# Kernel tuning notes

Measured on AMD Instinct MI355X. Metric: run time of the kernel, lower is better.

Reference implementation:

```python
import jax, jax.numpy as jnp
import numpy as np

B, DIM, H, W = 2, 512, 48, 48
HEADS = 8
HD = DIM // HEADS
NS = 7
R = NS // 2
SCALE = HD ** -0.5
EPS = 1e-12


def _proj(x, w, b):
    # 1x1 conv == channel linear: x [B,C,H,W], w [O,C], b [O]
    return jnp.einsum('bchw,oc->bohw', x, w) + b[None, :, None, None]


def _to_heads(t):
    # [B,C,H,W] -> [B,heads,H,W,head_dim]
    return t.reshape(B, HEADS, HD, H, W).transpose(0, 1, 3, 4, 2)


def setup_inputs() -> dict:
    key = jax.random.key(0)
    ks = jax.random.split(key, 9)
    std = DIM ** -0.5
    inp = {'x': jax.random.normal(ks[0], (B, DIM, H, W), jnp.float32)}
    names = ['wq', 'bq', 'wk', 'bk', 'wv', 'bv', 'wo', 'bo']
    for i, n in enumerate(names):
        if n.startswith('w'):
            inp[n] = jax.random.normal(ks[i + 1], (DIM, DIM), jnp.float32) * std
        else:
            inp[n] = jnp.zeros((DIM,), jnp.float32)
    return inp


def reference(x, wq, bq, wk, bk, wv, bv, wo, bo):
    q = _proj(x, wq, bq)
    k = _proj(x, wk, bk)
    v = _proj(x, wv, bv)
    qh, kh, vh = _to_heads(q), _to_heads(k), _to_heads(v)

    offs = jnp.arange(-R, R + 1)
    oy, ox = jnp.meshgrid(offs, offs, indexing='ij')
    oy, ox = oy.reshape(-1), ox.reshape(-1)  # [K]
    by, bx = jnp.meshgrid(jnp.arange(H), jnp.arange(W), indexing='ij')
    ny = by[..., None] + oy  # [H,W,K]
    nx = bx[..., None] + ox
    valid = (ny >= 0) & (ny < H) & (nx >= 0) & (nx < W)  # [H,W,K]
    ny = jnp.clip(ny, 0, H - 1)
    nx = jnp.clip(nx, 0, W - 1)

    K = NS * NS
    T = H * W
    # gather neighborhoods: [B,heads,H,W,K,head_dim]
    k_nb = kh[:, :, ny, nx].reshape(B, HEADS, T, K, HD)
    v_nb = vh[:, :, ny, nx].reshape(B, HEADS, T, K, HD)
    q_tok = qh.reshape(B, HEADS, T, HD)

    scores = jnp.einsum('bhtd,bhtkd->bhtk', q_tok, k_nb) * SCALE
    neg = jnp.finfo(scores.dtype).min
    scores = jnp.where(valid.reshape(1, 1, T, K), scores, neg)
    attn = jax.nn.softmax(scores, axis=-1)
    out = jnp.einsum('bhtk,bhtkd->bhtd', attn, v_nb)

    # exclude self-value component (self-attention path)
    sv = vh.reshape(B, HEADS, T, HD)
    sv_unit = sv / jnp.maximum(jnp.linalg.norm(sv, axis=-1, keepdims=True), EPS)
    out = out - (out * sv_unit).sum(-1, keepdims=True) * sv_unit

    # [B,heads,T,HD] -> [B,C,H,W]
    out = out.reshape(B, HEADS, H, W, HD).transpose(0, 1, 4, 2, 3).reshape(B, DIM, H, W)
    return _proj(out, wo, bo)
```

## Files before the change

### kernel.cpp

```cpp
#include <hip/hip_runtime.h>
#include <hip/hip_bf16.h>
#include <math.h>

typedef __hip_bfloat16 bf16;
typedef __attribute__((ext_vector_type(4))) float f32x4;
typedef __attribute__((ext_vector_type(8))) short s16x8;
typedef __attribute__((ext_vector_type(4))) short s16x4;

#define B_     2
#define DIM_   512
#define Hh     48
#define Ww     48
#define T_     2304
#define HEADS_ 8
#define HD_    64
#define NS_    7
#define R_     3
#define KK_    49

#define LDSTR  40

__device__ __forceinline__ short f2bs(float f) {
    bf16 h = __float2bfloat16(f);
    return *(short*)&h;
}

__device__ __forceinline__ s16x8 cvt8(const float* __restrict__ p) {
    f32x4 a = *(const f32x4*)p;
    f32x4 b = *(const f32x4*)(p + 4);
    s16x8 r;
    r[0] = f2bs(a[0]); r[1] = f2bs(a[1]); r[2] = f2bs(a[2]); r[3] = f2bs(a[3]);
    r[4] = f2bs(b[0]); r[5] = f2bs(b[1]); r[6] = f2bs(b[2]); r[7] = f2bs(b[3]);
    return r;
}

__global__ __launch_bounds__(256) void wcvt(
    const float* __restrict__ wq, const float* __restrict__ wk,
    const float* __restrict__ wv, const float* __restrict__ wo,
    bf16* __restrict__ wb)
{
    const int i     = blockIdx.x * 256 + threadIdx.x;
    const int which = i >> 15;
    const int off   = (i & 32767) * 8;
    const float* src = (which == 0) ? wq : (which == 1) ? wk : (which == 2) ? wv : wo;
    *(s16x8*)((short*)wb + which * 262144 + off) = cvt8(src + off);
}

__global__ __launch_bounds__(256) void prep_xt(
    const float* __restrict__ x, bf16* __restrict__ xt)
{
    __shared__ short tile[64 * 72];
    const int t0 = blockIdx.x * 64;
    const int c0 = blockIdx.y * 64;
    const int b  = blockIdx.z;
    const int tid = threadIdx.x;

    const float* X = x + (size_t)b * DIM_ * T_;

    const int c_l = tid >> 4;
    const int t4  = (tid & 15) * 4;
#pragma unroll
    for (int cp = 0; cp < 4; ++cp) {
        const int c = cp * 16 + c_l;
        f32x4 v = *(const f32x4*)(X + (size_t)(c0 + c) * T_ + t0 + t4);
#pragma unroll
        for (int e = 0; e < 4; ++e) tile[(t4 + e) * 72 + c] = f2bs(v[e]);
    }
    __syncthreads();

    const int t_l = tid >> 2;
    const int c16 = (tid & 3) * 16;
    short* dst = (short*)xt + ((size_t)b * T_ + t0 + t_l) * DIM_ + c0 + c16;
    *(s16x8*)(dst)     = *(const s16x8*)(&tile[t_l * 72 + c16]);
    *(s16x8*)(dst + 8) = *(const s16x8*)(&tile[t_l * 72 + c16 + 8]);
}

__global__ __launch_bounds__(256) void gemm_qkv(
    const bf16* __restrict__ xt, const bf16* __restrict__ wb,
    const float* __restrict__ bq, const float* __restrict__ bk,
    const float* __restrict__ bv,
    bf16* __restrict__ qb2, bf16* __restrict__ kb2,
    float* __restrict__ vtf, bf16* __restrict__ vb2)
{
    const int tt   = blockIdx.x * 128;
    const int ot   = blockIdx.y * 64;
    const int b    = blockIdx.z;
    const int proj = ot >> 9;
    const int orow = ot & 511;
    const int head = orow >> 6;

    const float* bsel = (proj == 0) ? bq : (proj == 1) ? bk : bv;
    const short* Wb   = (const short*)wb + proj * 262144;

    const short* X = (const short*)xt + (size_t)b * T_ * DIM_;

    __shared__ __align__(16) short Xs[128 * LDSTR];
    __shared__ __align__(16) short Ws[64 * LDSTR];

    const int tid  = threadIdx.x;
    const int lane = tid & 63;
    const int wid  = tid >> 6;

    const int row = tid >> 2;
    const int cq  = (tid & 3) * 8;

    f32x4 acc[2][4];
#pragma unroll
    for (int r = 0; r < 2; ++r)
#pragma unroll
        for (int n = 0; n < 4; ++n) acc[r][n] = (f32x4){0.f, 0.f, 0.f, 0.f};

    for (int kk = 0; kk < DIM_; kk += 32) {
#pragma unroll
        for (int rr = 0; rr < 2; ++rr)
            *(s16x8*)(&Xs[(rr * 64 + row) * LDSTR + cq]) =
                *(const s16x8*)(X + (size_t)(tt + rr * 64 + row) * DIM_ + kk + cq);
        *(s16x8*)(&Ws[row * LDSTR + cq]) =
            *(const s16x8*)(Wb + (size_t)(orow + row) * DIM_ + kk + cq);
        __syncthreads();

        s16x8 a[2];
#pragma unroll
        for (int r = 0; r < 2; ++r)
            a[r] = *(const s16x8*)(&Xs[(r * 64 + wid * 16 + (lane & 15)) * LDSTR + 8 * (lane >> 4)]);
#pragma unroll
        for (int n = 0; n < 4; ++n) {
            s16x8 bf = *(const s16x8*)(&Ws[(n * 16 + (lane & 15)) * LDSTR + 8 * (lane >> 4)]);
#pragma unroll
            for (int r = 0; r < 2; ++r)
                acc[r][n] = __builtin_amdgcn_mfma_f32_16x16x32_bf16(a[r], bf, acc[r][n], 0, 0, 0);
        }
        __syncthreads();
    }

    const size_t hb = (size_t)(b * HEADS_ + head) * T_ * HD_;
    if (proj < 2) {
        short* ob = (short*)(proj == 0 ? qb2 : kb2) + hb;
#pragma unroll
        for (int r = 0; r < 2; ++r)
#pragma unroll
            for (int n = 0; n < 4; ++n) {
                const int d    = n * 16 + (lane & 15);
                const float bi = bsel[orow + d];
#pragma unroll
                for (int e = 0; e < 4; ++e) {
                    const int t = tt + r * 64 + wid * 16 + (lane >> 4) * 4 + e;
                    ob[(size_t)t * HD_ + d] = f2bs(acc[r][n][e] + bi);
                }
            }
    } else {
        float* of = vtf + hb;
        short* ob = (short*)vb2 + hb;
#pragma unroll
        for (int r = 0; r < 2; ++r)
#pragma unroll
            for (int n = 0; n < 4; ++n) {
                const int d    = n * 16 + (lane & 15);
                const float bi = bsel[orow + d];
#pragma unroll
                for (int e = 0; e < 4; ++e) {
                    const int t = tt + r * 64 + wid * 16 + (lane >> 4) * 4 + e;
                    const float vv = acc[r][n][e] + bi;
                    of[(size_t)t * HD_ + d] = vv;
                    ob[(size_t)t * HD_ + d] = f2bs(vv);
                }
            }
    }
}

__global__ __launch_bounds__(256) void gemm_out(
    const bf16* __restrict__ ao, const bf16* __restrict__ wb,
    const float* __restrict__ bo, float* __restrict__ out)
{
    const int tt = blockIdx.x * 64;
    const int ot = blockIdx.y * 64;
    const int b  = blockIdx.z;

    const short* X  = (const short*)ao + (size_t)b * T_ * DIM_;
    const short* Wb = (const short*)wb + 3 * 262144;

    __shared__ __align__(16) short Ws[64 * LDSTR];
    __shared__ __align__(16) short Xs[64 * LDSTR];

    const int tid  = threadIdx.x;
    const int lane = tid & 63;
    const int wid  = tid >> 6;

    const int row = tid >> 2;
    const int cq  = (tid & 3) * 8;

    f32x4 acc[4];
#pragma unroll
    for (int n = 0; n < 4; ++n) acc[n] = (f32x4){0.f, 0.f, 0.f, 0.f};

    for (int kk = 0; kk < DIM_; kk += 32) {
        *(s16x8*)(&Ws[row * LDSTR + cq]) =
            *(const s16x8*)(Wb + (size_t)(ot + row) * DIM_ + kk + cq);
        *(s16x8*)(&Xs[row * LDSTR + cq]) =
            *(const s16x8*)(X + (size_t)(tt + row) * DIM_ + kk + cq);
        __syncthreads();

        s16x8 a = *(const s16x8*)(&Ws[(wid * 16 + (lane & 15)) * LDSTR + 8 * (lane >> 4)]);
#pragma unroll
        for (int n = 0; n < 4; ++n) {
            s16x8 bf = *(const s16x8*)(&Xs[(n * 16 + (lane & 15)) * LDSTR + 8 * (lane >> 4)]);
            acc[n] = __builtin_amdgcn_mfma_f32_16x16x32_bf16(a, bf, acc[n], 0, 0, 0);
        }
        __syncthreads();
    }

    float* obase = out + (size_t)b * DIM_ * T_;
#pragma unroll
    for (int n = 0; n < 4; ++n) {
        const int t = tt + n * 16 + (lane & 15);
#pragma unroll
        for (int e = 0; e < 4; ++e) {
            const int o    = ot + wid * 16 + (lane >> 4) * 4 + e;
            obase[(size_t)o * T_ + t] = acc[n][e] + bo[o];
        }
    }
}

__global__ __launch_bounds__(256, 4) void attn_mfma(
    const bf16* __restrict__ qb2, const bf16* __restrict__ kb2,
    const float* __restrict__ vtf, const bf16* __restrict__ vb2,
    bf16* __restrict__ ao)
{
    __shared__ __align__(16) char smem[34048];
    short* Kl = (short*)smem;
    short* Ql = (short*)(smem + 25344);
    short* VT = (short*)smem;
    short* Pl = (short*)(smem + 27648);
    float* Ol = (float*)(smem + 27648);

    const int l   = blockIdx.x;
    const int idx = (l & 7) * 288 + (l >> 3);
    const int bh  = idx / 144;
    const int rem = idx - bh * 144;
    const int y   = rem / 3;
    const int x0  = (rem % 3) * 16;

    const short* qb  = (const short*)qb2 + (size_t)bh * T_ * HD_;
    const short* kb  = (const short*)kb2 + (size_t)bh * T_ * HD_;
    const short* vbb = (const short*)vb2 + (size_t)bh * T_ * HD_;
    const float* vbf = vtf + (size_t)bh * T_ * HD_;

    const int tid  = threadIdx.x;
    const int lane = tid & 63;
    const int wv   = tid >> 6;
    const int qq   = lane >> 4;
    const int ln   = lane & 15;

    if (tid < 32) {
        const int t = tid >> 1, c = tid & 1;
        *(s16x8*)&Pl[t * 200 + 176 + c * 8] = (s16x8){0,0,0,0,0,0,0,0};
    }
    {
        const int c8 = (tid & 7) * 8;
        const int wr = tid >> 3;
#pragma unroll
        for (int p = 0; p < 6; ++p) {
            const int w = p * 32 + wr;
            if (w < 168) {
                const int wy = w / 24, u = w - wy * 24;
                if (u < 22) {
                    const int gy = min(max(y + wy - 3, 0), 47);
                    const int gx = min(max(x0 + u - 3, 0), 47);
                    *(s16x8*)&Kl[w * 72 + c8] =
                        *(const s16x8*)(kb + (size_t)(gy * 48 + gx) * 64 + c8);
                }
            }
        }
    }
    if (tid < 128) {
        const int t = tid >> 3, c8 = (tid & 7) * 8;
        *(s16x8*)&Ql[t * 72 + c8] =
            *(const s16x8*)(qb + (size_t)(y * 48 + x0 + t) * 64 + c8);
    }
    s16x4 vreg[10];
    {
        const int rr0 = tid >> 4;
        const int d4  = (tid & 15) * 4;
#pragma unroll
        for (int p = 0; p < 10; ++p) {
            const int rr = p * 16 + rr0;
            if (rr < 154) {
                const int wy = rr / 22, u = rr - wy * 22;
                const int gy = min(max(y + wy - 3, 0), 47);
                const int gx = min(max(x0 + u - 3, 0), 47);
                vreg[p] = *(const s16x4*)(vbb + (size_t)(gy * 48 + gx) * 64 + d4);
            }
        }
    }
    __syncthreads();

    f32x4 acc[11];
#pragma unroll
    for (int mt = 0; mt < 11; ++mt) acc[mt] = (f32x4){0.f, 0.f, 0.f, 0.f};
#pragma unroll
    for (int ks = 0; ks < 2; ++ks) {
        s16x8 bq_ = *(const s16x8*)&Ql[ln * 72 + ks * 32 + qq * 8];
#pragma unroll
        for (int mt = 0; mt < 11; ++mt) {
            s16x8 ak = *(const s16x8*)&Kl[(mt * 16 + ln) * 72 + ks * 32 + qq * 8];
            acc[mt] = __builtin_amdgcn_mfma_f32_16x16x32_bf16(ak, bq_, acc[mt], 0, 0, 0);
        }
    }

    const int dx = ln;
    float mxv = -3.0e38f;
#pragma unroll
    for (int mt = 0; mt < 11; ++mt) {
#pragma unroll
        for (int e = 0; e < 4; ++e) {
            const int w  = mt * 16 + qq * 4 + e;
            const int wy = w / 24, u = w - wy * 24;
            const bool valid = (w < 168) &&
                               ((unsigned)(u - dx) <= 6u) &&
                               ((unsigned)(y + wy - 3) < 48u) &&
                               ((unsigned)(x0 + u - 3) < 48u);
            const float s = valid ? acc[mt][e] * 0.125f : -3.0e38f;
            acc[mt][e] = s;
            mxv = fmaxf(mxv, s);
        }
    }
    mxv = fmaxf(mxv, __shfl_xor(mxv, 16));
    mxv = fmaxf(mxv, __shfl_xor(mxv, 32));
    float sum = 0.f;
#pragma unroll
    for (int mt = 0; mt < 11; ++mt)
#pragma unroll
        for (int e = 0; e < 4; ++e) {
            const float p = __expf(acc[mt][e] - mxv);
            acc[mt][e] = p;
            sum += p;
        }
    sum += __shfl_xor(sum, 16);
    sum += __shfl_xor(sum, 32);
    const float inv = 1.0f / sum;

#pragma unroll
    for (int mt = 0; mt < 11; ++mt) {
        const int owner = (mt >= 9) ? 3 : (mt / 3);
        if (wv == owner) {
#pragma unroll
            for (int e = 0; e < 4; ++e) {
                const int w = mt * 16 + qq * 4 + e;
                Pl[ln * 200 + w] = f2bs(acc[mt][e] * inv);
            }
        }
    }
    __syncthreads();

    {
        const int d = tid >> 2, c = tid & 3;
        *(s16x8*)&VT[d * 200 + 168 + c * 8] = (s16x8){0,0,0,0,0,0,0,0};
    }
#pragma unroll
    for (int pp = 0; pp < 2; ++pp) {
        const int r2 = pp * 256 + tid;
        if (r2 < 448) {
            const int wy = r2 >> 6, d = r2 & 63;
            *(unsigned*)&VT[d * 200 + wy * 24 + 22] = 0u;
        }
    }
    {
        const int rr0 = tid >> 4;
        const int d4  = (tid & 15) * 4;
        const int rot = tid & 3;
#pragma unroll
        for (int p = 0; p < 10; ++p) {
            const int rr = p * 16 + rr0;
            if (rr < 154) {
                const int wy = rr / 22, u = rr - wy * 22;
                const int w  = wy * 24 + u;
#pragma unroll
                for (int e = 0; e < 4; ++e) {
                    const int ee = (e + rot) & 3;
                    VT[(d4 + ee) * 200 + w] = vreg[p][ee];
                }
            }
        }
    }
    __syncthreads();

    f32x4 oacc = (f32x4){0.f, 0.f, 0.f, 0.f};
#pragma unroll
    for (int ks = 0; ks < 6; ++ks) {
        s16x8 ap  = *(const s16x8*)&Pl[ln * 200 + ks * 32 + qq * 8];
        s16x8 bv_ = *(const s16x8*)&VT[(wv * 16 + ln) * 200 + ks * 32 + qq * 8];
        oacc = __builtin_amdgcn_mfma_f32_16x16x32_bf16(ap, bv_, oacc, 0, 0, 0);
    }
    __syncthreads();
#pragma unroll
    for (int e = 0; e < 4; ++e)
        Ol[(qq * 4 + e) * 72 + wv * 16 + ln] = oacc[e];
    __syncthreads();

    {
        const int tt = tid >> 4;
        const int dl = tid & 15;
        const int tg = y * 48 + x0 + tt;
        const float o0 = Ol[tt * 72 + dl],      o1 = Ol[tt * 72 + dl + 16],
                    o2 = Ol[tt * 72 + dl + 32], o3 = Ol[tt * 72 + dl + 48];
        const float* vs = vbf + (size_t)tg * 64 + dl;
        const float v0 = vs[0], v1 = vs[16], v2 = vs[32], v3 = vs[48];
        float n2  = v0 * v0 + v1 * v1 + v2 * v2 + v3 * v3;
        float odv = o0 * v0 + o1 * v1 + o2 * v2 + o3 * v3;
#pragma unroll
        for (int off = 1; off < 16; off <<= 1) {
            n2  += __shfl_xor(n2, off);
            odv += __shfl_xor(odv, off);
        }
        const float mxn = fmaxf(sqrtf(n2), 1e-12f);
        const float cf  = odv / (mxn * mxn);
        const int b = bh >> 3, h = bh & 7;
        bf16* dst = ao + ((size_t)b * T_ + tg) * DIM_ + h * 64 + dl;
        dst[0]  = __float2bfloat16(o0 - cf * v0);
        dst[16] = __float2bfloat16(o1 - cf * v1);
        dst[32] = __float2bfloat16(o2 - cf * v2);
        dst[48] = __float2bfloat16(o3 - cf * v3);
    }
}

extern "C" void kernel_launch(void* const* d_in, const int* in_sizes, int n_in,
                              void* d_out, int out_size, void* d_ws, size_t ws_size,
                              hipStream_t stream)
{
    (void)in_sizes; (void)n_in; (void)out_size; (void)ws_size;

    const float* x  = (const float*)d_in[0];
    const float* wq = (const float*)d_in[1];
    const float* bq = (const float*)d_in[2];
    const float* wk = (const float*)d_in[3];
    const float* bk = (const float*)d_in[4];
    const float* wv = (const float*)d_in[5];
    const float* bv = (const float*)d_in[6];
    const float* wo = (const float*)d_in[7];
    const float* bo = (const float*)d_in[8];
    float* out = (float*)d_out;

    const size_t per = (size_t)B_ * HEADS_ * T_ * HD_;
    float* vtf = (float*)d_ws;
    bf16*  qb2 = (bf16*)(vtf + per);
    bf16*  kb2 = qb2 + per;
    bf16*  vb2 = kb2 + per;
    bf16*  xa  = vb2 + per;
    bf16*  wb  = xa + per;

    wcvt<<<dim3(512), 256, 0, stream>>>(wq, wk, wv, wo, wb);
    prep_xt<<<dim3(T_ / 64, DIM_ / 64, B_), 256, 0, stream>>>(x, xa);

    dim3 g1(T_ / 128, 1536 / 64, B_);
    gemm_qkv<<<g1, 256, 0, stream>>>(xa, wb, bq, bk, bv, qb2, kb2, vtf, vb2);

    attn_mfma<<<dim3(B_ * HEADS_ * (T_ / 16)), 256, 0, stream>>>(qb2, kb2, vtf, vb2, xa);

    dim3 g2(T_ / 64, DIM_ / 64, B_);
    gemm_out<<<g2, 256, 0, stream>>>(xa, wb, bo, out);
}
```

Baseline: 70.25 us.

## Merge prep kernels, widen QKV GEMM tile, drop fp32 V copy

Merges the weight-conversion and x-transpose kernels into one launch that splits work by block index. The QKV GEMM output tile grows from 64 to 128 channels (two heads per block), which halves the grid and doubles per-block accumulators, aiming for more reuse of the X tile. The fp32 V buffer is removed, and the attention epilogue reads the bf16 V copy for the self-value projection. This cuts write and read traffic at some precision cost in the self-exclusion term, and the larger tile raises register pressure while leaving fewer blocks to fill the GPU.

```diff
diff --git a/kernel.cpp b/kernel.cpp
--- a/kernel.cpp
+++ b/kernel.cpp
@@ -25,6 +25,11 @@
     return *(short*)&h;
 }
 
+__device__ __forceinline__ float bs2f(short s) {
+    bf16 h = *reinterpret_cast<const bf16*>(&s);
+    return __bfloat162float(h);
+}
+
 __device__ __forceinline__ s16x8 cvt8(const float* __restrict__ p) {
     f32x4 a = *(const f32x4*)p;
     f32x4 b = *(const f32x4*)(p + 4);
@@ -34,26 +39,31 @@
     return r;
 }
 
-__global__ __launch_bounds__(256) void wcvt(
+__global__ __launch_bounds__(256) void prep(
+    const float* __restrict__ x,
     const float* __restrict__ wq, const float* __restrict__ wk,
     const float* __restrict__ wv, const float* __restrict__ wo,
-    bf16* __restrict__ wb)
-{
-    const int i     = blockIdx.x * 256 + threadIdx.x;
-    const int which = i >> 15;
-    const int off   = (i & 32767) * 8;
-    const float* src = (which == 0) ? wq : (which == 1) ? wk : (which == 2) ? wv : wo;
-    *(s16x8*)((short*)wb + which * 262144 + off) = cvt8(src + off);
-}
-
-__global__ __launch_bounds__(256) void prep_xt(
-    const float* __restrict__ x, bf16* __restrict__ xt)
+    bf16* __restrict__ xt, bf16* __restrict__ wb)
 {
     __shared__ short tile[64 * 72];
-    const int t0 = blockIdx.x * 64;
-    const int c0 = blockIdx.y * 64;
-    const int b  = blockIdx.z;
+    const int gid = blockIdx.x;
     const int tid = threadIdx.x;
+
+    if (gid < 512) {
+        const int i     = gid * 256 + tid;
+        const int which = i >> 15;
+        const int off   = (i & 32767) * 8;
+        const float* src = (which == 0) ? wq : (which == 1) ? wk
+                         : (which == 2) ? wv : wo;
+        *(s16x8*)((short*)wb + which * 262144 + off) = cvt8(src + off);
+        return;
+    }
+
+    const int pid = gid - 512;
+    const int b   = pid / 288;
+    const int rem = pid - b * 288;
+    const int t0  = (rem % 36) * 64;
+    const int c0  = (rem / 36) * 64;
 
     const float* X = x + (size_t)b * DIM_ * T_;
 
@@ -79,53 +89,54 @@
     const bf16* __restrict__ xt, const bf16* __restrict__ wb,
     const float* __restrict__ bq, const float* __restrict__ bk,
     const float* __restrict__ bv,
-    bf16* __restrict__ qb2, bf16* __restrict__ kb2,
-    float* __restrict__ vtf, bf16* __restrict__ vb2)
+    bf16* __restrict__ qb2, bf16* __restrict__ kb2, bf16* __restrict__ vb2)
 {
     const int tt   = blockIdx.x * 128;
-    const int ot   = blockIdx.y * 64;
+    const int ot   = blockIdx.y * 128;
     const int b    = blockIdx.z;
     const int proj = ot >> 9;
     const int orow = ot & 511;
-    const int head = orow >> 6;
+    const int h0   = orow >> 6;
 
     const float* bsel = (proj == 0) ? bq : (proj == 1) ? bk : bv;
     const short* Wb   = (const short*)wb + proj * 262144;
-
-    const short* X = (const short*)xt + (size_t)b * T_ * DIM_;
+    const short* X    = (const short*)xt + (size_t)b * T_ * DIM_;
+    short*       sel  = (short*)((proj == 0) ? qb2 : (proj == 1) ? kb2 : vb2);
 
     __shared__ __align__(16) short Xs[128 * LDSTR];
-    __shared__ __align__(16) short Ws[64 * LDSTR];
+    __shared__ __align__(16) short Ws[128 * LDSTR];
 
     const int tid  = threadIdx.x;
     const int lane = tid & 63;
     const int wid  = tid >> 6;
+    const int ln   = lane & 15;
 
     const int row = tid >> 2;
     const int cq  = (tid & 3) * 8;
 
-    f32x4 acc[2][4];
+    f32x4 acc[2][8];
 #pragma unroll
     for (int r = 0; r < 2; ++r)
 #pragma unroll
-        for (int n = 0; n < 4; ++n) acc[r][n] = (f32x4){0.f, 0.f, 0.f, 0.f};
+        for (int n = 0; n < 8; ++n) acc[r][n] = (f32x4){0.f, 0.f, 0.f, 0.f};
 
     for (int kk = 0; kk < DIM_; kk += 32) {
 #pragma unroll
-        for (int rr = 0; rr < 2; ++rr)
+        for (int rr = 0; rr < 2; ++rr) {
             *(s16x8*)(&Xs[(rr * 64 + row) * LDSTR + cq]) =
                 *(const s16x8*)(X + (size_t)(tt + rr * 64 + row) * DIM_ + kk + cq);
-        *(s16x8*)(&Ws[row * LDSTR + cq]) =
-            *(const s16x8*)(Wb + (size_t)(orow + row) * DIM_ + kk + cq);
+            *(s16x8*)(&Ws[(rr * 64 + row) * LDSTR + cq]) =
+                *(const s16x8*)(Wb + (size_t)(orow + rr * 64 + row) * DIM_ + kk + cq);
+        }
         __syncthreads();
 
         s16x8 a[2];
 #pragma unroll
         for (int r = 0; r < 2; ++r)
-            a[r] = *(const s16x8*)(&Xs[(r * 64 + wid * 16 + (lane & 15)) * LDSTR + 8 * (lane >> 4)]);
-#pragma unroll
-        for (int n = 0; n < 4; ++n) {
-            s16x8 bf = *(const s16x8*)(&Ws[(n * 16 + (lane & 15)) * LDSTR + 8 * (lane >> 4)]);
+            a[r] = *(const s16x8*)(&Xs[(r * 64 + wid * 16 + ln) * LDSTR + 8 * (lane >> 4)]);
+#pragma unroll
+        for (int n = 0; n < 8; ++n) {
+            s16x8 bf = *(const s16x8*)(&Ws[(n * 16 + ln) * LDSTR + 8 * (lane >> 4)]);
 #pragma unroll
             for (int r = 0; r < 2; ++r)
                 acc[r][n] = __builtin_amdgcn_mfma_f32_16x16x32_bf16(a[r], bf, acc[r][n], 0, 0, 0);
@@ -133,39 +144,20 @@
         __syncthreads();
     }
 
-    const size_t hb = (size_t)(b * HEADS_ + head) * T_ * HD_;
-    if (proj < 2) {
-        short* ob = (short*)(proj == 0 ? qb2 : kb2) + hb;
-#pragma unroll
-        for (int r = 0; r < 2; ++r)
-#pragma unroll
-            for (int n = 0; n < 4; ++n) {
-                const int d    = n * 16 + (lane & 15);
-                const float bi = bsel[orow + d];
-#pragma unroll
-                for (int e = 0; e < 4; ++e) {
-                    const int t = tt + r * 64 + wid * 16 + (lane >> 4) * 4 + e;
-                    ob[(size_t)t * HD_ + d] = f2bs(acc[r][n][e] + bi);
-                }
+    const size_t tb = (size_t)(b * HEADS_ + h0);
+#pragma unroll
+    for (int r = 0; r < 2; ++r)
+#pragma unroll
+        for (int n = 0; n < 8; ++n) {
+            const int hn   = n >> 2;
+            const int d    = (n & 3) * 16 + ln;
+            const float bi = bsel[orow + n * 16 + ln];
+#pragma unroll
+            for (int e = 0; e < 4; ++e) {
+                const int t = tt + r * 64 + wid * 16 + (lane >> 4) * 4 + e;
+                sel[((tb + hn) * T_ + t) * HD_ + d] = f2bs(acc[r][n][e] + bi);
             }
-    } else {
-        float* of = vtf + hb;
-        short* ob = (short*)vb2 + hb;
-#pragma unroll
-        for (int r = 0; r < 2; ++r)
-#pragma unroll
-            for (int n = 0; n < 4; ++n) {
-                const int d    = n * 16 + (lane & 15);
-                const float bi = bsel[orow + d];
-#pragma unroll
-                for (int e = 0; e < 4; ++e) {
-                    const int t = tt + r * 64 + wid * 16 + (lane >> 4) * 4 + e;
-                    const float vv = acc[r][n][e] + bi;
-                    of[(size_t)t * HD_ + d] = vv;
-                    ob[(size_t)t * HD_ + d] = f2bs(vv);
-                }
-            }
-    }
+        }
 }
 
 __global__ __launch_bounds__(256) void gemm_out(
@@ -223,8 +215,7 @@
 
 __global__ __launch_bounds__(256, 4) void attn_mfma(
     const bf16* __restrict__ qb2, const bf16* __restrict__ kb2,
-    const float* __restrict__ vtf, const bf16* __restrict__ vb2,
-    bf16* __restrict__ ao)
+    const bf16* __restrict__ vb2, bf16* __restrict__ ao)
 {
     __shared__ __align__(16) char smem[34048];
     short* Kl = (short*)smem;
@@ -243,7 +234,6 @@
     const short* qb  = (const short*)qb2 + (size_t)bh * T_ * HD_;
     const short* kb  = (const short*)kb2 + (size_t)bh * T_ * HD_;
     const short* vbb = (const short*)vb2 + (size_t)bh * T_ * HD_;
-    const float* vbf = vtf + (size_t)bh * T_ * HD_;
 
     const int tid  = threadIdx.x;
     const int lane = tid & 63;
@@ -403,8 +393,9 @@
         const int tg = y * 48 + x0 + tt;
         const float o0 = Ol[tt * 72 + dl],      o1 = Ol[tt * 72 + dl + 16],
                     o2 = Ol[tt * 72 + dl + 32], o3 = Ol[tt * 72 + dl + 48];
-        const float* vs = vbf + (size_t)tg * 64 + dl;
-        const float v0 = vs[0], v1 = vs[16], v2 = vs[32], v3 = vs[48];
+        const short* vs = vbb + (size_t)tg * 64 + dl;
+        const float v0 = bs2f(vs[0]),  v1 = bs2f(vs[16]),
+                    v2 = bs2f(vs[32]), v3 = bs2f(vs[48]);
         float n2  = v0 * v0 + v1 * v1 + v2 * v2 + v3 * v3;
         float odv = o0 * v0 + o1 * v1 + o2 * v2 + o3 * v3;
 #pragma unroll
@@ -441,20 +432,18 @@
     float* out = (float*)d_out;
 
     const size_t per = (size_t)B_ * HEADS_ * T_ * HD_;
-    float* vtf = (float*)d_ws;
-    bf16*  qb2 = (bf16*)(vtf + per);
-    bf16*  kb2 = qb2 + per;
-    bf16*  vb2 = kb2 + per;
-    bf16*  xa  = vb2 + per;
-    bf16*  wb  = xa + per;
-
-    wcvt<<<dim3(512), 256, 0, stream>>>(wq, wk, wv, wo, wb);
-    prep_xt<<<dim3(T_ / 64, DIM_ / 64, B_), 256, 0, stream>>>(x, xa);
-
-    dim3 g1(T_ / 128, 1536 / 64, B_);
-    gemm_qkv<<<g1, 256, 0, stream>>>(xa, wb, bq, bk, bv, qb2, kb2, vtf, vb2);
-
-    attn_mfma<<<dim3(B_ * HEADS_ * (T_ / 16)), 256, 0, stream>>>(qb2, kb2, vtf, vb2, xa);
+    bf16* qb2 = (bf16*)d_ws;
+    bf16* kb2 = qb2 + per;
+    bf16* vb2 = kb2 + per;
+    bf16* xa  = vb2 + per;
+    bf16* wb  = xa + per;
+
+    prep<<<dim3(512 + 576), 256, 0, stream>>>(x, wq, wk, wv, wo, xa, wb);
+
+    dim3 g1(T_ / 128, 1536 / 128, B_);
+    gemm_qkv<<<g1, 256, 0, stream>>>(xa, wb, bq, bk, bv, qb2, kb2, vb2);
+
+    attn_mfma<<<dim3(B_ * HEADS_ * (T_ / 16)), 256, 0, stream>>>(qb2, kb2, vb2, xa);
 
     dim3 g2(T_ / 64, DIM_ / 64, B_);
     gemm_out<<<g2, 256, 0, stream>>>(xa, wb, bo, out);
```

New measurement: 66.03 us. 6.0% less time.
